# Performance work log

Hardware: AMD Instinct MI355X
Metric: run time of the kernel (lower is better)

The kernel has to match this reference:

```python
import jax, jax.numpy as jnp
import numpy as np

N = 50000
E = 800000
D_IN, D_HID, D_OUT = 256, 256, 128


def _xavier(key, shape):
    fan_in, fan_out = shape
    limit = float(np.sqrt(6.0 / (fan_in + fan_out)))
    return jax.random.uniform(key, shape, jnp.float32, -limit, limit)


def setup_inputs() -> dict:
    key = jax.random.key(0)
    ks = jax.random.split(key, 12)
    x = jax.random.normal(ks[0], (N, D_IN), jnp.float32)
    edge_index = jax.random.randint(ks[1], (2, E), 0, N, dtype=jnp.int64)
    batch = jnp.zeros((N,), jnp.int64)
    # per-layer: message weight W, linear weight LW (stored [in, out]), bias b
    w1 = _xavier(ks[2], (D_IN, D_HID))
    lw1 = _xavier(ks[3], (D_IN, D_HID))
    lb1 = jnp.zeros((D_HID,), jnp.float32)
    w2 = _xavier(ks[4], (D_HID, D_HID))
    lw2 = _xavier(ks[5], (D_HID, D_HID))
    lb2 = jnp.zeros((D_HID,), jnp.float32)
    w3 = _xavier(ks[6], (D_HID, D_OUT))
    lw3 = _xavier(ks[7], (D_HID, D_OUT))
    lb3 = jnp.zeros((D_OUT,), jnp.float32)
    return {"x": x, "edge_index": edge_index, "batch": batch,
            "w1": w1, "lw1": lw1, "lb1": lb1,
            "w2": w2, "lw2": lw2, "lb2": lb2,
            "w3": w3, "lw3": lw3, "lb3": lb3}


def _gcn_layer(x, W, LW, b, row, col, norm):
    # message: norm * (x_j @ W); equivalent and cheaper: transform nodes once, gather
    xw = x @ W                                   # [N, out]
    msg = norm[:, None] * xw[row]                # [E, out]
    agg = jax.ops.segment_sum(msg, col, num_segments=x.shape[0])  # scatter-add at col
    return agg + x @ LW + b                      # residual linear path


def reference(x, edge_index, batch, w1, lw1, lb1, w2, lw2, lb2, w3, lw3, lb3):
    row, col = edge_index[0], edge_index[1]
    ones = jnp.ones((row.shape[0],), x.dtype)
    out_deg = jax.ops.segment_sum(ones, row, num_segments=N)
    in_deg = jax.ops.segment_sum(ones, col, num_segments=N)
    # inf at zero-degree nodes never gets gathered (those nodes have no edges)
    norm = out_deg[row] ** -0.5 * in_deg[col] ** -0.5  # [E]

    h = jax.nn.relu(_gcn_layer(x, w1, lw1, lb1, row, col, norm))
    h = jax.nn.relu(_gcn_layer(h, w2, lw2, lb2, row, col, norm))
    h = jax.nn.sigmoid(_gcn_layer(h, w3, lw3, lb3, row, col, norm))
    return h
```

## Files before the change

### kernel.cpp

```cpp
#include <hip/hip_runtime.h>
#include <hip/hip_bf16.h>
#include <math.h>

#define NNODES 50000
#define NEDGES 800000
#define HNB 128
#define HBINS 50176
#define SCAN_NB 196

typedef short s8v __attribute__((ext_vector_type(8)));
typedef float f4v __attribute__((ext_vector_type(4)));
using bf16 = __hip_bfloat16;

static __device__ __forceinline__ float bflo(unsigned int x) {
    union { unsigned int i; float f; } c; c.i = x << 16; return c.f;
}
static __device__ __forceinline__ float bfhi(unsigned int x) {
    union { unsigned int i; float f; } c; c.i = x & 0xffff0000u; return c.f;
}


__global__ void k_packb(const float* __restrict__ W, const float* __restrict__ LW,
                        bf16* __restrict__ out, int K, int C) {
    int i = blockIdx.x * blockDim.x + threadIdx.x;
    int C2 = 2 * C;
    if (i >= K * C2) return;
    int k = i / C2, j = i % C2;
    float v = (j < C) ? W[k * C + j] : LW[k * C + (j - C)];
    out[i] = __float2bfloat16(v);
}


__global__ __launch_bounds__(256) void k_hist(const int* __restrict__ ei, ushort* __restrict__ partials) {
    __shared__ unsigned int h32[HBINS / 2];
    int b = blockIdx.x, row = blockIdx.y, t = threadIdx.x;
    for (int i = t; i < HBINS / 2; i += 256) h32[i] = 0;
    __syncthreads();
    const int chunk = NEDGES / HNB;
    int beg = b * chunk, end = beg + chunk;
    const int* p = ei + (size_t)row * NEDGES;
    for (int e = beg + t; e < end; e += 256) {
        int id = p[e];
        atomicAdd(&h32[id >> 1], 1u << (16 * (id & 1)));
    }
    __syncthreads();
    unsigned int* o32 = (unsigned int*)(partials + ((size_t)row * HNB + b) * HBINS);
    for (int i = t; i < HBINS / 2; i += 256) o32[i] = h32[i];
}

__global__ __launch_bounds__(256) void k_hist_reduce(const ushort* __restrict__ partials,
                                                     float* __restrict__ rsqrt_out,
                                                     int* __restrict__ in_cnt,
                                                     int* __restrict__ block_sums) {
    __shared__ int sm[256];
    int row = blockIdx.y;
    int i = blockIdx.x * 256 + threadIdx.x;
    const ushort* p = partials + (size_t)row * HNB * HBINS + i;
    int s = 0;
#pragma unroll 4
    for (int b = 0; b < HNB; ++b) s += p[(size_t)b * HBINS];
    if (row == 0) {
        if (i < NNODES) rsqrt_out[i] = rsqrtf((float)s);
    } else {
        if (i < NNODES) in_cnt[i] = s;
        sm[threadIdx.x] = s;
        __syncthreads();
        for (int off = 128; off > 0; off >>= 1) {
            if (threadIdx.x < off) sm[threadIdx.x] += sm[threadIdx.x + off];
            __syncthreads();
        }
        if (threadIdx.x == 0) block_sums[blockIdx.x] = sm[0];
    }
}


__global__ void k_scan_blocks(const int* __restrict__ block_sums, int* __restrict__ block_base, int nb) {
    __shared__ int s[256];
    int t = threadIdx.x;
    int v = (t < nb) ? block_sums[t] : 0;
    s[t] = v;
    __syncthreads();
    for (int off = 1; off < 256; off <<= 1) {
        int u = (t >= off) ? s[t - off] : 0;
        __syncthreads();
        s[t] += u;
        __syncthreads();
    }
    block_base[t] = s[t] - v;
}

__global__ void k_scan_final(const int* __restrict__ in_cnt, const int* __restrict__ block_base,
                             int* __restrict__ offsets, int* __restrict__ cursor) {
    __shared__ int s[256];
    int b = blockIdx.x, t = threadIdx.x;
    int i = b * 256 + t;
    int v = (i < NNODES) ? in_cnt[i] : 0;
    s[t] = v;
    __syncthreads();
    for (int off = 1; off < 256; off <<= 1) {
        int u = (t >= off) ? s[t - off] : 0;
        __syncthreads();
        s[t] += u;
        __syncthreads();
    }
    int excl = s[t] - v + block_base[b];
    if (i < NNODES) { offsets[i] = excl; cursor[i] = excl; }
    if (i == NNODES - 1) offsets[NNODES] = excl + v;
}

__global__ void k_scatter(const int* __restrict__ ei, int* __restrict__ cursor,
                          int* __restrict__ src_sorted) {
    int e = blockIdx.x * blockDim.x + threadIdx.x;
    if (e < NEDGES) {
        int r = ei[e], c = ei[NEDGES + e];
        int p = atomicAdd(&cursor[c], 1);
        src_sorted[p] = r;
    }
}

template<int D, int C2, int ACT>
__global__ __launch_bounds__(64) void k_agg_fused(const bf16* __restrict__ xwcat,
                                                  const int* __restrict__ offsets,
                                                  const int* __restrict__ src_sorted,
                                                  const float* __restrict__ rsqrt_out,
                                                  const float* __restrict__ bias,
                                                  void* __restrict__ out) {
    const int L = D / 8;
    const int G = 64 / L;
    const int U = 4;
    int lane = threadIdx.x;
    int v = blockIdx.x;
    int g = lane / L, sl = lane % L;

    int beg = offsets[v], end = offsets[v + 1];
    int deg = end - beg;
    int dcap = min(deg, 64);

    int id = 0; float wl = 0.f;
    if (lane < dcap) {
        id = src_sorted[beg + lane];
        wl = rsqrt_out[id];
    }

    float acc[U][8];
#pragma unroll
    for (int u = 0; u < U; ++u)
#pragma unroll
        for (int c = 0; c < 8; ++c) acc[u][c] = 0.f;

    const ushort* base = (const ushort*)xwcat + sl * 8;

    for (int e0 = 0; e0 < dcap; e0 += G * U) {
#pragma unroll
        for (int u = 0; u < U; ++u) {
            int e = e0 + u * G + g;
            int s = __shfl(id, e & 63, 64);
            float w = __shfl(wl, e & 63, 64);
            if (e >= dcap) w = 0.f;
            uint4 q = *(const uint4*)(base + (size_t)s * C2);
            acc[u][0] += w * bflo(q.x); acc[u][1] += w * bfhi(q.x);
            acc[u][2] += w * bflo(q.y); acc[u][3] += w * bfhi(q.y);
            acc[u][4] += w * bflo(q.z); acc[u][5] += w * bfhi(q.z);
            acc[u][6] += w * bflo(q.w); acc[u][7] += w * bfhi(q.w);
        }
    }
    for (int j = beg + 64 + g; j < end; j += G) {
        int s = src_sorted[j];
        float w = rsqrt_out[s];
        uint4 q = *(const uint4*)(base + (size_t)s * C2);
        acc[0][0] += w * bflo(q.x); acc[0][1] += w * bfhi(q.x);
        acc[0][2] += w * bflo(q.y); acc[0][3] += w * bfhi(q.y);
        acc[0][4] += w * bflo(q.z); acc[0][5] += w * bfhi(q.z);
        acc[0][6] += w * bflo(q.w); acc[0][7] += w * bfhi(q.w);
    }

#pragma unroll
    for (int c = 0; c < 8; ++c) acc[0][c] = (acc[0][c] + acc[1][c]) + (acc[2][c] + acc[3][c]);
#pragma unroll
    for (int d = 32; d >= L; d >>= 1) {
#pragma unroll
        for (int c = 0; c < 8; ++c) acc[0][c] += __shfl_down(acc[0][c], d, 64);
    }

    if (lane < L) {
        float sc = (deg > 0) ? rsqrtf((float)deg) : 0.f;
        const ushort* lwp = (const ushort*)xwcat + (size_t)v * C2 + D + sl * 8;
        uint4 ql = *(const uint4*)lwp;
        const float* bp = bias + sl * 8;
        float4 b0 = *(const float4*)bp, b1 = *(const float4*)(bp + 4);
        float h[8];
        h[0] = acc[0][0] * sc + bflo(ql.x) + b0.x;
        h[1] = acc[0][1] * sc + bfhi(ql.x) + b0.y;
        h[2] = acc[0][2] * sc + bflo(ql.y) + b0.z;
        h[3] = acc[0][3] * sc + bfhi(ql.y) + b0.w;
        h[4] = acc[0][4] * sc + bflo(ql.z) + b1.x;
        h[5] = acc[0][5] * sc + bfhi(ql.z) + b1.y;
        h[6] = acc[0][6] * sc + bflo(ql.w) + b1.z;
        h[7] = acc[0][7] * sc + bfhi(ql.w) + b1.w;
        if (ACT == 1) {
            union { bf16 hh[8]; uint4 u; } o;
#pragma unroll
            for (int c = 0; c < 8; ++c) o.hh[c] = __float2bfloat16(fmaxf(h[c], 0.f));
            *(uint4*)((ushort*)out + (size_t)v * D + sl * 8) = o.u;
        } else {
            float r[8];
#pragma unroll
            for (int c = 0; c < 8; ++c) r[c] = 1.f / (1.f + expf(-h[c]));
            float* op = (float*)out + (size_t)v * D + sl * 8;
            *(float4*)op = (float4){r[0], r[1], r[2], r[3]};
            *(float4*)(op + 4) = (float4){r[4], r[5], r[6], r[7]};
        }
    }
}

template<int C2, bool A_BF16>
__global__ __launch_bounds__(256) void k_gemm_fused(const void* __restrict__ Aptr,
                                                    const bf16* __restrict__ B,
                                                    bf16* __restrict__ Out) {
    __shared__ bf16 As[64][40];
    __shared__ bf16 Bs[128][40];
    const int R = NNODES;
    int t = threadIdx.x;
    int wave = t >> 6, lane = t & 63;
    int r0 = blockIdx.x * 64;
    int n0 = blockIdx.y * 128;

    f4v acc[8];
#pragma unroll
    for (int i = 0; i < 8; ++i) acc[i] = (f4v){0.f, 0.f, 0.f, 0.f};

    int arow = t >> 2, aseg = t & 3;
    int bn = t & 127, bhalf = t >> 7;

    for (int k0 = 0; k0 < 256; k0 += 32) {
        {
            union { bf16 h[8]; uint4 v; } u;
            int gr = r0 + arow;
            if (gr < R) {
                if (A_BF16) {
                    const bf16* Ab = (const bf16*)Aptr;
                    u.v = *(const uint4*)(Ab + (size_t)gr * 256 + k0 + aseg * 8);
                } else {
                    const float* Af = (const float*)Aptr;
                    const float4* p = (const float4*)(Af + (size_t)gr * 256 + k0 + aseg * 8);
                    float4 f0 = p[0], f1 = p[1];
                    u.h[0] = __float2bfloat16(f0.x); u.h[1] = __float2bfloat16(f0.y);
                    u.h[2] = __float2bfloat16(f0.z); u.h[3] = __float2bfloat16(f0.w);
                    u.h[4] = __float2bfloat16(f1.x); u.h[5] = __float2bfloat16(f1.y);
                    u.h[6] = __float2bfloat16(f1.z); u.h[7] = __float2bfloat16(f1.w);
                }
            } else {
                u.v = (uint4){0, 0, 0, 0};
            }
            *(uint4*)&As[arow][aseg * 8] = u.v;
        }
        {
#pragma unroll
            for (int s8 = 0; s8 < 2; ++s8) {
                int kseg = bhalf * 2 + s8;
                union { bf16 h[8]; uint4 v; } u;
#pragma unroll
                for (int j = 0; j < 8; ++j)
                    u.h[j] = B[(size_t)(k0 + kseg * 8 + j) * C2 + n0 + bn];
                *(uint4*)&Bs[bn][kseg * 8] = u.v;
            }
        }
        __syncthreads();
        int m = wave * 16 + (lane & 15);
        int kq = (lane >> 4) * 8;
        s8v a = *(const s8v*)&As[m][kq];
#pragma unroll
        for (int nt = 0; nt < 8; ++nt) {
            s8v b = *(const s8v*)&Bs[nt * 16 + (lane & 15)][kq];
            acc[nt] = __builtin_amdgcn_mfma_f32_16x16x32_bf16(a, b, acc[nt], 0, 0, 0);
        }
        __syncthreads();
    }
#pragma unroll
    for (int nt = 0; nt < 8; ++nt) {
#pragma unroll
        for (int r = 0; r < 4; ++r) {
            int grow = r0 + wave * 16 + (lane >> 4) * 4 + r;
            int gcol = n0 + nt * 16 + (lane & 15);
            if (grow < R)
                Out[(size_t)grow * C2 + gcol] = __float2bfloat16(acc[nt][r]);
        }
    }
}


extern "C" void kernel_launch(void* const* d_in, const int* in_sizes, int n_in,
                              void* d_out, int out_size, void* d_ws, size_t ws_size,
                              hipStream_t stream) {
    const float* x   = (const float*)d_in[0];
    const int*   ei  = (const int*)d_in[1];
    const float* w1  = (const float*)d_in[3];
    const float* lw1 = (const float*)d_in[4];
    const float* lb1 = (const float*)d_in[5];
    const float* w2  = (const float*)d_in[6];
    const float* lw2 = (const float*)d_in[7];
    const float* lb2 = (const float*)d_in[8];
    const float* w3  = (const float*)d_in[9];
    const float* lw3 = (const float*)d_in[10];
    const float* lb3 = (const float*)d_in[11];
    float* out = (float*)d_out;

    char* ws = (char*)d_ws;
    size_t off = 0;
    auto alloc = [&](size_t bytes) -> void* {
        void* p = ws + off;
        off += (bytes + 255) & ~(size_t)255;
        return p;
    };
    int*    in_cnt     = (int*)alloc((size_t)HBINS * 4);
    float*  rsqrt_out  = (float*)alloc((size_t)HBINS * 4);
    int*    offsets    = (int*)alloc((size_t)(NNODES + 1) * 4);
    int*    cursor     = (int*)alloc((size_t)NNODES * 4);
    int*    block_sums = (int*)alloc((size_t)256 * 4);
    int*    block_base = (int*)alloc((size_t)256 * 4);
    ushort* partials   = (ushort*)alloc((size_t)2 * HNB * HBINS * 2);
    int*    src_sorted = (int*)alloc((size_t)NEDGES * 4);
    bf16*   wcat1      = (bf16*)alloc((size_t)256 * 512 * 2);
    bf16*   wcat2      = (bf16*)alloc((size_t)256 * 512 * 2);
    bf16*   wcat3      = (bf16*)alloc((size_t)256 * 256 * 2);
    bf16*   xwcat      = (bf16*)alloc((size_t)NNODES * 512 * 2);
    bf16*   h1         = (bf16*)alloc((size_t)NNODES * 256 * 2);
    bf16*   h2         = (bf16*)alloc((size_t)NNODES * 256 * 2);

    k_packb<<<512, 256, 0, stream>>>(w1, lw1, wcat1, 256, 256);
    k_packb<<<512, 256, 0, stream>>>(w2, lw2, wcat2, 256, 256);
    k_packb<<<256, 256, 0, stream>>>(w3, lw3, wcat3, 256, 128);

    k_hist<<<dim3(HNB, 2), 256, 0, stream>>>(ei, partials);
    k_hist_reduce<<<dim3(SCAN_NB, 2), 256, 0, stream>>>(partials, rsqrt_out, in_cnt, block_sums);
    k_scan_blocks<<<1, 256, 0, stream>>>(block_sums, block_base, SCAN_NB);
    k_scan_final<<<SCAN_NB, 256, 0, stream>>>(in_cnt, block_base, offsets, cursor);
    int eblocks = (NEDGES + 255) / 256;
    k_scatter<<<eblocks, 256, 0, stream>>>(ei, cursor, src_sorted);

    int gx = (NNODES + 63) / 64;

    k_gemm_fused<512, false><<<dim3(gx, 4), 256, 0, stream>>>(x, wcat1, xwcat);
    k_agg_fused<256, 512, 1><<<NNODES, 64, 0, stream>>>(xwcat, offsets, src_sorted, rsqrt_out, lb1, h1);
    k_gemm_fused<512, true><<<dim3(gx, 4), 256, 0, stream>>>(h1, wcat2, xwcat);
    k_agg_fused<256, 512, 1><<<NNODES, 64, 0, stream>>>(xwcat, offsets, src_sorted, rsqrt_out, lb2, h2);
    k_gemm_fused<256, true><<<dim3(gx, 2), 256, 0, stream>>>(h2, wcat3, xwcat);
    k_agg_fused<128, 256, 2><<<NNODES, 64, 0, stream>>>(xwcat, offsets, src_sorted, rsqrt_out, lb3, out);
}
```

Before: 442.7 us.

## Rewrite GEMM with 128x128 tiles, transposed weights, LDS direct loads, XCD-aware mapping

Pre-transposes the concatenated weight matrices so B tiles load as contiguous 16-byte rows instead of strided scalar gathers. The GEMM moves from 64x128 tiles with one MFMA row per wave to 128x128 tiles with a 2x2 wave grid, each wave computing 4x4 MFMA blocks for more register reuse. bf16 A and B tiles are loaded with global_load_lds straight into LDS. Blocks are remapped so consecutive tiles land on the same XCD for L2 locality. The larger tiles raise register pressure and halve block count, and the LDS layout has no padding, so bank conflicts may appear.

```diff
diff --git a/kernel.cpp b/kernel.cpp
--- a/kernel.cpp
+++ b/kernel.cpp
@@ -19,14 +19,20 @@
     union { unsigned int i; float f; } c; c.i = x & 0xffff0000u; return c.f;
 }
 
-
-__global__ void k_packb(const float* __restrict__ W, const float* __restrict__ LW,
-                        bf16* __restrict__ out, int K, int C) {
+static __device__ __forceinline__ void gload16(const void* g, void* l) {
+    __builtin_amdgcn_global_load_lds(
+        (const __attribute__((address_space(1))) unsigned int*)g,
+        (__attribute__((address_space(3))) unsigned int*)l, 16, 0, 0);
+}
+
+
+__global__ void k_packbt(const float* __restrict__ W, const float* __restrict__ LW,
+                         bf16* __restrict__ out, int K, int C) {
     int i = blockIdx.x * blockDim.x + threadIdx.x;
     int C2 = 2 * C;
     if (i >= K * C2) return;
-    int k = i / C2, j = i % C2;
-    float v = (j < C) ? W[k * C + j] : LW[k * C + (j - C)];
+    int n = i / K, k = i % K;
+    float v = (n < C) ? W[k * C + n] : LW[k * C + (n - C)];
     out[i] = __float2bfloat16(v);
 }
 
@@ -214,76 +220,97 @@
 }
 
 template<int C2, bool A_BF16>
-__global__ __launch_bounds__(256) void k_gemm_fused(const void* __restrict__ Aptr,
-                                                    const bf16* __restrict__ B,
-                                                    bf16* __restrict__ Out) {
-    __shared__ bf16 As[64][40];
-    __shared__ bf16 Bs[128][40];
-    const int R = NNODES;
+__global__ __launch_bounds__(256) void k_gemm2(const void* __restrict__ Aptr,
+                                               const bf16* __restrict__ BT,
+                                               bf16* __restrict__ Out) {
+    constexpr int R = NNODES;
+    constexpr int GX = (NNODES + 127) / 128;
+    constexpr int GY = C2 / 128;
+    constexpr int NWG = GX * GY;
+    __shared__ bf16 As[128 * 32];
+    __shared__ bf16 Bs[128 * 32];
+
+    int o = blockIdx.x;
+    constexpr int qq = NWG / 8, rr = NWG % 8;
+    int xcd = o & 7, idx = o >> 3;
+    int lt = (xcd < rr ? xcd * (qq + 1) : rr * (qq + 1) + (xcd - rr) * qq) + idx;
+    int r0 = (lt / GY) * 128;
+    int n0 = (lt % GY) * 128;
+
     int t = threadIdx.x;
     int wave = t >> 6, lane = t & 63;
-    int r0 = blockIdx.x * 64;
-    int n0 = blockIdx.y * 128;
-
-    f4v acc[8];
-#pragma unroll
-    for (int i = 0; i < 8; ++i) acc[i] = (f4v){0.f, 0.f, 0.f, 0.f};
-
-    int arow = t >> 2, aseg = t & 3;
-    int bn = t & 127, bhalf = t >> 7;
+    int wr = wave >> 1, wc = wave & 1;
+
+    f4v acc[4][4];
+#pragma unroll
+    for (int mi = 0; mi < 4; ++mi)
+#pragma unroll
+        for (int ni = 0; ni < 4; ++ni) acc[mi][ni] = (f4v){0.f, 0.f, 0.f, 0.f};
+
+    int sr = t >> 2;
+    int sk = (t & 3) * 8;
+    int fr = t >> 1, fs = (t & 1) * 16;
 
     for (int k0 = 0; k0 < 256; k0 += 32) {
-        {
-            union { bf16 h[8]; uint4 v; } u;
-            int gr = r0 + arow;
-            if (gr < R) {
-                if (A_BF16) {
-                    const bf16* Ab = (const bf16*)Aptr;
-                    u.v = *(const uint4*)(Ab + (size_t)gr * 256 + k0 + aseg * 8);
-                } else {
-                    const float* Af = (const float*)Aptr;
-                    const float4* p = (const float4*)(Af + (size_t)gr * 256 + k0 + aseg * 8);
-                    float4 f0 = p[0], f1 = p[1];
-                    u.h[0] = __float2bfloat16(f0.x); u.h[1] = __float2bfloat16(f0.y);
-                    u.h[2] = __float2bfloat16(f0.z); u.h[3] = __float2bfloat16(f0.w);
-                    u.h[4] = __float2bfloat16(f1.x); u.h[5] = __float2bfloat16(f1.y);
-                    u.h[6] = __float2bfloat16(f1.z); u.h[7] = __float2bfloat16(f1.w);
+        if (A_BF16) {
+            const bf16* Ab = (const bf16*)Aptr;
+            gload16(Ab + (size_t)min(r0 + sr, R - 1) * 256 + k0 + sk,
+                    (char*)As + wave * 1024);
+            gload16(Ab + (size_t)min(r0 + sr + 64, R - 1) * 256 + k0 + sk,
+                    (char*)As + 4096 + wave * 1024);
+        } else {
+            const float* Af = (const float*)Aptr + (size_t)min(r0 + fr, R - 1) * 256 + k0 + fs;
+            float4 f0 = ((const float4*)Af)[0];
+            float4 f1 = ((const float4*)Af)[1];
+            float4 f2 = ((const float4*)Af)[2];
+            float4 f3 = ((const float4*)Af)[3];
+            union { bf16 h[16]; uint4 u[2]; } cv;
+            cv.h[0]  = __float2bfloat16(f0.x); cv.h[1]  = __float2bfloat16(f0.y);
+            cv.h[2]  = __float2bfloat16(f0.z); cv.h[3]  = __float2bfloat16(f0.w);
+            cv.h[4]  = __float2bfloat16(f1.x); cv.h[5]  = __float2bfloat16(f1.y);
+            cv.h[6]  = __float2bfloat16(f1.z); cv.h[7]  = __float2bfloat16(f1.w);
+            cv.h[8]  = __float2bfloat16(f2.x); cv.h[9]  = __float2bfloat16(f2.y);
+            cv.h[10] = __float2bfloat16(f2.z); cv.h[11] = __float2bfloat16(f2.w);
+            cv.h[12] = __float2bfloat16(f3.x); cv.h[13] = __float2bfloat16(f3.y);
+            cv.h[14] = __float2bfloat16(f3.z); cv.h[15] = __float2bfloat16(f3.w);
+            *(uint4*)&As[fr * 32 + fs]     = cv.u[0];
+            *(uint4*)&As[fr * 32 + fs + 8] = cv.u[1];
+        }
+        gload16(BT + (size_t)(n0 + sr) * 256 + k0 + sk,
+                (char*)Bs + wave * 1024);
+        gload16(BT + (size_t)(n0 + sr + 64) * 256 + k0 + sk,
+                (char*)Bs + 4096 + wave * 1024);
+        __syncthreads();
+
+        int lr = lane & 15, lk = (lane >> 4) * 8;
+        s8v a[4], b[4];
+#pragma unroll
+        for (int mi = 0; mi < 4; ++mi)
+            a[mi] = *(const s8v*)&As[(wr * 64 + mi * 16 + lr) * 32 + lk];
+#pragma unroll
+        for (int ni = 0; ni < 4; ++ni)
+            b[ni] = *(const s8v*)&Bs[(wc * 64 + ni * 16 + lr) * 32 + lk];
+#pragma unroll
+        for (int mi = 0; mi < 4; ++mi)
+#pragma unroll
+            for (int ni = 0; ni < 4; ++ni)
+                acc[mi][ni] = __builtin_amdgcn_mfma_f32_16x16x32_bf16(a[mi], b[ni], acc[mi][ni], 0, 0, 0);
+        __syncthreads();
+    }
+
+    int lr = lane & 15, lq = (lane >> 4) * 4;
+#pragma unroll
+    for (int mi = 0; mi < 4; ++mi) {
+#pragma unroll
+        for (int rj = 0; rj < 4; ++rj) {
+            int grow = r0 + wr * 64 + mi * 16 + lq + rj;
+            if (grow < R) {
+#pragma unroll
+                for (int ni = 0; ni < 4; ++ni) {
+                    Out[(size_t)grow * C2 + n0 + wc * 64 + ni * 16 + lr] =
+                        __float2bfloat16(acc[mi][ni][rj]);
                 }
-            } else {
-                u.v = (uint4){0, 0, 0, 0};
             }
-            *(uint4*)&As[arow][aseg * 8] = u.v;
-        }
-        {
-#pragma unroll
-            for (int s8 = 0; s8 < 2; ++s8) {
-                int kseg = bhalf * 2 + s8;
-                union { bf16 h[8]; uint4 v; } u;
-#pragma unroll
-                for (int j = 0; j < 8; ++j)
-                    u.h[j] = B[(size_t)(k0 + kseg * 8 + j) * C2 + n0 + bn];
-                *(uint4*)&Bs[bn][kseg * 8] = u.v;
-            }
-        }
-        __syncthreads();
-        int m = wave * 16 + (lane & 15);
-        int kq = (lane >> 4) * 8;
-        s8v a = *(const s8v*)&As[m][kq];
-#pragma unroll
-        for (int nt = 0; nt < 8; ++nt) {
-            s8v b = *(const s8v*)&Bs[nt * 16 + (lane & 15)][kq];
-            acc[nt] = __builtin_amdgcn_mfma_f32_16x16x32_bf16(a, b, acc[nt], 0, 0, 0);
-        }
-        __syncthreads();
-    }
-#pragma unroll
-    for (int nt = 0; nt < 8; ++nt) {
-#pragma unroll
-        for (int r = 0; r < 4; ++r) {
-            int grow = r0 + wave * 16 + (lane >> 4) * 4 + r;
-            int gcol = n0 + nt * 16 + (lane & 15);
-            if (grow < R)
-                Out[(size_t)grow * C2 + gcol] = __float2bfloat16(acc[nt][r]);
         }
     }
 }
@@ -327,9 +354,9 @@
     bf16*   h1         = (bf16*)alloc((size_t)NNODES * 256 * 2);
     bf16*   h2         = (bf16*)alloc((size_t)NNODES * 256 * 2);
 
-    k_packb<<<512, 256, 0, stream>>>(w1, lw1, wcat1, 256, 256);
-    k_packb<<<512, 256, 0, stream>>>(w2, lw2, wcat2, 256, 256);
-    k_packb<<<256, 256, 0, stream>>>(w3, lw3, wcat3, 256, 128);
+    k_packbt<<<512, 256, 0, stream>>>(w1, lw1, wcat1, 256, 256);
+    k_packbt<<<512, 256, 0, stream>>>(w2, lw2, wcat2, 256, 256);
+    k_packbt<<<256, 256, 0, stream>>>(w3, lw3, wcat3, 256, 128);
 
     k_hist<<<dim3(HNB, 2), 256, 0, stream>>>(ei, partials);
     k_hist_reduce<<<dim3(SCAN_NB, 2), 256, 0, stream>>>(partials, rsqrt_out, in_cnt, block_sums);
@@ -338,12 +365,10 @@
     int eblocks = (NEDGES + 255) / 256;
     k_scatter<<<eblocks, 256, 0, stream>>>(ei, cursor, src_sorted);
 
-    int gx = (NNODES + 63) / 64;
-
-    k_gemm_fused<512, false><<<dim3(gx, 4), 256, 0, stream>>>(x, wcat1, xwcat);
+    k_gemm2<512, false><<<391 * 4, 256, 0, stream>>>(x, wcat1, xwcat);
     k_agg_fused<256, 512, 1><<<NNODES, 64, 0, stream>>>(xwcat, offsets, src_sorted, rsqrt_out, lb1, h1);
-    k_gemm_fused<512, true><<<dim3(gx, 4), 256, 0, stream>>>(h1, wcat2, xwcat);
+    k_gemm2<512, true><<<391 * 4, 256, 0, stream>>>(h1, wcat2, xwcat);
     k_agg_fused<256, 512, 1><<<NNODES, 64, 0, stream>>>(xwcat, offsets, src_sorted, rsqrt_out, lb2, h2);
-    k_gemm_fused<256, true><<<dim3(gx, 2), 256, 0, stream>>>(h2, wcat3, xwcat);
+    k_gemm2<256, true><<<391 * 2, 256, 0, stream>>>(h2, wcat3, xwcat);
     k_agg_fused<128, 256, 2><<<NNODES, 64, 0, stream>>>(xwcat, offsets, src_sorted, rsqrt_out, lb3, out);
 }
```

After: 430.3 us. 1.03x faster.
